# Kernel optimization log

Hardware: AMD Instinct MI355X
Metric: run time of the kernel (lower is better)

Reference implementation:

```python
import jax, jax.numpy as jnp
import numpy as np

DEPTH = 256
HEADS = 8
K = 128          # kernel_size == attended axis length (height)
DH = DEPTH // HEADS  # 32
EPS = 1e-5


def _bn(x, gamma, beta, axes):
    # training-mode batch norm (biased variance), per-channel on axis 1
    mean = jnp.mean(x, axis=axes, keepdims=True)
    var = jnp.var(x, axis=axes, keepdims=True)
    shape = [1] * x.ndim
    shape[1] = x.shape[1]
    g = gamma.reshape(shape)
    b = beta.reshape(shape)
    return (x - mean) * jax.lax.rsqrt(var + EPS) * g + b


def setup_inputs() -> dict:
    key = jax.random.key(0)
    ks = jax.random.split(key, 3)
    x = jax.random.normal(ks[0], (2, DEPTH, K, K), dtype=jnp.float32)
    w_kqv = jax.random.normal(ks[1], (2 * DEPTH, DEPTH), dtype=jnp.float32) * 0.05
    rel_encoding = jax.random.normal(ks[2], (2 * DH, 2 * K - 1), dtype=jnp.float32)
    return {
        "x": x,
        "w_kqv": w_kqv,
        "kqv_gamma": jnp.ones((2 * DEPTH,), jnp.float32),
        "kqv_beta": jnp.zeros((2 * DEPTH,), jnp.float32),
        "logits_gamma": jnp.ones((3 * HEADS,), jnp.float32),
        "logits_beta": jnp.zeros((3 * HEADS,), jnp.float32),
        "rel_encoding": rel_encoding,
    }


def reference(x, w_kqv, kqv_gamma, kqv_beta, logits_gamma, logits_beta, rel_encoding):
    B, C, H, W = x.shape  # height_dim=True path
    # (B,C,H,W) -> (B,W,C,H) -> (B*W, C, H)
    xf = jnp.transpose(x, (0, 3, 1, 2)).reshape(B * W, C, H)
    # 1x1 conv == channel matmul
    kqv = jnp.einsum('oc,bch->boh', w_kqv, xf)  # (BW, 2*depth, H)
    kqv = _bn(kqv, kqv_gamma, kqv_beta, axes=(0, 2))
    kqv = kqv.reshape(B * W, HEADS, 2 * DH, H)
    k = kqv[:, :, : DH // 2]            # (BW, h, dh/2, H)
    q = kqv[:, :, DH // 2: DH]          # (BW, h, dh/2, H)
    v = kqv[:, :, DH:]                  # (BW, h, dh,   H)

    # relative position gather: (2*dh, 2K-1) -> (2*dh, K, K)
    idx = (jnp.arange(K)[None, :] - jnp.arange(K)[:, None] + K - 1).reshape(-1)
    rel = rel_encoding[:, idx].reshape(2 * DH, K, K)
    q_enc = rel[: DH // 2]
    k_enc = rel[DH // 2: DH]
    v_enc = rel[DH:]

    qk = jnp.einsum('bhdx,bhdy->bhxy', q, k)
    qr = jnp.einsum('bhdx,dxy->bhxy', q, q_enc)
    kr = jnp.swapaxes(jnp.einsum('bhdx,dxy->bhxy', k, k_enc), 2, 3)
    logits = jnp.concatenate([qk, qr, kr], axis=1)  # (BW, 3*h, K, K)
    logits = _bn(logits, logits_gamma, logits_beta, axes=(0, 2, 3))
    logits = logits.reshape(B * W, 3, HEADS, H, H).sum(axis=1)
    weights = jax.nn.softmax(logits, axis=3)  # (BW, h, K, K)

    attn = jnp.einsum('bhxy,bhdy->bhdx', weights, v)         # (BW, h, dh, H)
    attn_enc = jnp.einsum('bhxy,dxy->bhdx', weights, v_enc)  # (BW, h, dh, H)
    out = (attn + attn_enc).reshape(B, W, DEPTH, H)  # cat+reshape+sum(dim=-2) == add
    out = jnp.transpose(out, (0, 2, 3, 1))  # (B, depth, H, W)
    return out
```

## Files before the change

kernel.cpp:

```cpp
#include <hip/hip_runtime.h>
#include <hip/hip_bf16.h>

#define H 128
#define NB 256
#define OC 512
#define CIN 256
#define NN 16384
#define EPS 1e-5f

#define EQG_OFF 524288
#define EKG_OFF 589824
#define EVG_OFF 655360

typedef __attribute__((ext_vector_type(4))) float f32x4;
typedef __attribute__((ext_vector_type(8))) short bf16x8;
typedef unsigned short u16x8 __attribute__((ext_vector_type(8)));

__device__ __forceinline__ float bf2f(unsigned short u){
    return __uint_as_float(((unsigned int)u) << 16);
}
__device__ __forceinline__ unsigned short f2bf(float f){
    unsigned int x = __float_as_uint(f);
    return (unsigned short)((x + 0x7fffu + ((x >> 16) & 1u)) >> 16);
}
__device__ __forceinline__ float ldin(const void* p, size_t i, bool f32){
    return f32 ? ((const float*)p)[i] : bf2f(((const unsigned short*)p)[i]);
}
__device__ __forceinline__ short ld_bf16(const void* p, size_t i, bool f32){
    if (f32) return (short)f2bf(((const float*)p)[i]);
    return ((const short*)p)[i];
}
__device__ __forceinline__ bool probe_f32(const void* gamma_ones){
    return *(const unsigned int*)gamma_ones == 0x3F800000u;
}

template<bool F32>
__device__ __forceinline__ void gemm_body(const void* __restrict__ w,
                                          const void* __restrict__ x,
                                          unsigned short* __restrict__ c1,
                                          short (*As)[128][40], short (*Bs)[64][40])
{
    const int m0 = blockIdx.x * 128;
    const int n0 = blockIdx.y * 64;
    const int b0 = blockIdx.z;
    const int t  = threadIdx.x;
    const int lane = t & 63, wv = t >> 6;
    const int wm = wv & 1, wn = wv >> 1;
    const int lm = lane & 15, quad = lane >> 4;
    const size_t xb = (size_t)b0 * CIN * NN;
    const int am = t >> 1, ak = (t & 1) * 16;
    const int bn = t & 63, bk = (t >> 6) * 8;

    float4 pa[4]; float pb[8];
    u16x8 qa[2]; unsigned short qb[8];

    auto load_tile = [&](int k0){
        if constexpr (F32){
            const float* wp = (const float*)w + (size_t)(m0+am)*CIN + k0 + ak;
            #pragma unroll
            for (int q=0;q<4;q++) pa[q] = *(const float4*)(wp + 4*q);
            const float* xp = (const float*)x + xb + (size_t)(k0+bk)*NN + n0 + bn;
            #pragma unroll
            for (int i=0;i<8;i++) pb[i] = xp[(size_t)i*NN];
        } else {
            const unsigned short* wp = (const unsigned short*)w + (size_t)(m0+am)*CIN + k0 + ak;
            qa[0] = *(const u16x8*)wp; qa[1] = *(const u16x8*)(wp+8);
            const unsigned short* xp = (const unsigned short*)x + xb + (size_t)(k0+bk)*NN + n0 + bn;
            #pragma unroll
            for (int i=0;i<8;i++) qb[i] = xp[(size_t)i*NN];
        }
    };
    auto store_tile = [&](int buf){
        if constexpr (F32){
            short ta[16];
            #pragma unroll
            for (int q=0;q<4;q++){
                ta[4*q+0]=(short)f2bf(pa[q].x); ta[4*q+1]=(short)f2bf(pa[q].y);
                ta[4*q+2]=(short)f2bf(pa[q].z); ta[4*q+3]=(short)f2bf(pa[q].w);
            }
            *(bf16x8*)&As[buf][am][ak]   = *(bf16x8*)&ta[0];
            *(bf16x8*)&As[buf][am][ak+8] = *(bf16x8*)&ta[8];
            #pragma unroll
            for (int i=0;i<8;i++) Bs[buf][bn][bk+i] = (short)f2bf(pb[i]);
        } else {
            *(u16x8*)&As[buf][am][ak]   = qa[0];
            *(u16x8*)&As[buf][am][ak+8] = qa[1];
            #pragma unroll
            for (int i=0;i<8;i++) Bs[buf][bn][bk+i] = (short)qb[i];
        }
    };

    f32x4 acc[4][2];
    #pragma unroll
    for (int i=0;i<4;i++){ acc[i][0]=(f32x4){0,0,0,0}; acc[i][1]=(f32x4){0,0,0,0}; }

    load_tile(0); store_tile(0); __syncthreads();
    for (int kk=0; kk<8; ++kk){
        const int cur = kk & 1;
        if (kk < 7) load_tile((kk+1)*32);
        bf16x8 af[4], bfB[2];
        #pragma unroll
        for (int i=0;i<4;i++) af[i]  = *(const bf16x8*)&As[cur][wm*64 + i*16 + lm][quad*8];
        #pragma unroll
        for (int j=0;j<2;j++) bfB[j] = *(const bf16x8*)&Bs[cur][wn*32 + j*16 + lm][quad*8];
        #pragma unroll
        for (int i=0;i<4;i++)
            #pragma unroll
            for (int j=0;j<2;j++)
                acc[i][j] = __builtin_amdgcn_mfma_f32_16x16x32_bf16(af[i], bfB[j], acc[i][j], 0,0,0);
        if (kk < 7) store_tile(cur ^ 1);
        __syncthreads();
    }
    #pragma unroll
    for (int i=0;i<4;i++){
        #pragma unroll
        for (int j=0;j<2;j++){
            int n = n0 + wn*32 + j*16 + lm;
            #pragma unroll
            for (int r=0;r<4;r++){
                int m = m0 + wm*64 + i*16 + quad*4 + r;
                c1[((size_t)b0*OC + m)*NN + n] = f2bf(acc[i][j][r]);
            }
        }
    }
}

__global__ __launch_bounds__(256) void k_gemm(const void* __restrict__ w,
                                              const void* __restrict__ x,
                                              unsigned short* __restrict__ c1,
                                              const void* __restrict__ probe)
{
    __shared__ short As[2][128][40];
    __shared__ short Bs[2][64][40];
    if (probe_f32(probe)) gemm_body<true >(w, x, c1, As, Bs);
    else                  gemm_body<false>(w, x, c1, As, Bs);
}

__global__ __launch_bounds__(256) void k_bn_transpose(const unsigned short* __restrict__ c1,
        unsigned short* __restrict__ kqvt,
        const void* __restrict__ gamma, const void* __restrict__ beta)
{
    __shared__ float T[128][129];
    __shared__ float red[8];
    __shared__ float sc_sh[2];
    const bool f32 = probe_f32(gamma);
    const int o = blockIdx.x;
    const int t = threadIdx.x;
    const int lane = t & 63, wv = t >> 6;
    const unsigned short* r0 = c1 + (size_t)o*NN;
    const unsigned short* r1 = c1 + ((size_t)OC + o)*NN;
    const u16x8* r08 = (const u16x8*)r0;
    const u16x8* r18 = (const u16x8*)r1;
    float s=0.f, ss=0.f;
    #pragma unroll
    for (int i=0;i<8;i++){
        u16x8 a = r08[t + i*256];
        u16x8 b = r18[t + i*256];
        #pragma unroll
        for (int e=0;e<8;e++){
            float va = bf2f(a[e]); s += va; ss = fmaf(va,va,ss);
            float vb = bf2f(b[e]); s += vb; ss = fmaf(vb,vb,ss);
        }
    }
    #pragma unroll
    for (int off=1; off<64; off<<=1){ s += __shfl_xor(s,off); ss += __shfl_xor(ss,off); }
    if (lane==0){ red[wv*2] = s; red[wv*2+1] = ss; }
    __syncthreads();
    if (t==0){
        float st=0.f, sq=0.f;
        for (int i=0;i<4;i++){ st += red[i*2]; sq += red[i*2+1]; }
        float mean = st * (1.f/32768.f);
        float var  = sq * (1.f/32768.f) - mean*mean;
        float scale = ldin(gamma, o, f32) * rsqrtf(var + EPS);
        sc_sh[0] = scale;
        sc_sh[1] = ldin(beta, o, f32) - mean*scale;
    }
    __syncthreads();
    const float scale = sc_sh[0], shift = sc_sh[1];
    for (int b0=0;b0<2;b0++){
        const unsigned short* r = b0 ? r1 : r0;
        for (int i=0;i<64;i++){
            int idx = t + i*256;
            int h = idx >> 7, ww = idx & 127;
            T[ww][h] = fmaf(bf2f(r[idx]), scale, shift);
        }
        __syncthreads();
        for (int i=0;i<64;i++){
            int idx = t + i*256;
            int ww = idx >> 7, h = idx & 127;
            kqvt[(((size_t)(b0*128 + ww))*OC + o)*H + h] = f2bf(T[ww][h]);
        }
        __syncthreads();
    }
}

__global__ __launch_bounds__(256) void k_encpre(const void* __restrict__ relenc,
        float* __restrict__ ws, const void* __restrict__ probe)
{
    __shared__ float E[16][256];
    const bool f32 = probe_f32(probe);
    const int grp = blockIdx.x;
    const int t = threadIdx.x;
    if (grp == 2){
        unsigned short* ev = (unsigned short*)ws + EVG_OFF;
        for (int i = t; i < 32*264; i += 256){
            int d = i / 264, j = i - d*264;
            ev[i] = (j < 255) ? (unsigned short)ld_bf16(relenc, (size_t)(32+d)*255 + j, f32) : 0;
        }
        return;
    }
    for (int i = t; i < 16*255; i += 256){
        int d = i / 255, j = i - d*255;
        E[d][j] = bf2f((unsigned short)ld_bf16(relenc, (size_t)(grp*16 + d)*255 + j, f32));
    }
    __syncthreads();
    float* Rout = ws + 256  + grp*2048;
    float* Cout = ws + 8192 + grp*32768;
    {
        const int d = t >> 4, e = t & 15;
        const float* Ed = E[d]; const float* Ee = E[e];
        float c = 0.f;
        for (int j = 0; j < 128; ++j) c = fmaf(Ed[j], Ee[j], c);
        float* Cp = Cout + (d*16+e)*128;
        Cp[127] = c;
        for (int xx = 126; xx >= 0; --xx){
            c += Ed[254-xx]*Ee[254-xx] - Ed[126-xx]*Ee[126-xx];
            Cp[xx] = c;
        }
    }
    if (t < 16){
        const float* Ed = E[t];
        float r = 0.f;
        for (int j = 0; j < 128; ++j) r += Ed[j];
        float* Rp = Rout + t*128;
        Rp[127] = r;
        for (int xx = 126; xx >= 0; --xx){
            r += Ed[254-xx] - Ed[126-xx];
            Rp[xx] = r;
        }
    }
}

__global__ __launch_bounds__(256) void k_stats2(const unsigned short* __restrict__ kqvt,
        const float* __restrict__ ws, float* __restrict__ stats)
{
    __shared__ short QK[2][16][128];
    __shared__ float wr[4][6];
    const int b = blockIdx.x >> 3, head = blockIdx.x & 7;
    const int t = threadIdx.x;
    const int lane = t & 63, wv = t >> 6;
    const int lm = lane & 15, quad = lane >> 4;
    const unsigned short* base = kqvt + ((size_t)b*OC + head*64)*H;
    for (int i = t; i < 512; i += 256){
        int arr = i >> 8, d = (i >> 4) & 15, c = i & 15;
        *(u16x8*)&QK[arr][d][c*8] = *(const u16x8*)&base[(size_t)(arr*16 + d)*H + c*8];
    }
    __syncthreads();

    float s_qk = 0.f, q_qk = 0.f;
    if (wv == 0){
        f32x4 gq  = (f32x4){0,0,0,0}, gk  = (f32x4){0,0,0,0};
        f32x4 gq1 = (f32x4){0,0,0,0}, gk1 = (f32x4){0,0,0,0};
        bf16x8 ones;
        #pragma unroll
        for (int i=0;i<8;i++) ones[i] = (short)0x3F80;
        #pragma unroll
        for (int xt=0; xt<4; ++xt){
            bf16x8 fq = *(const bf16x8*)&QK[1][lm][xt*32 + quad*8];
            bf16x8 fk = *(const bf16x8*)&QK[0][lm][xt*32 + quad*8];
            gq  = __builtin_amdgcn_mfma_f32_16x16x32_bf16(fq, fq,   gq,  0,0,0);
            gk  = __builtin_amdgcn_mfma_f32_16x16x32_bf16(fk, fk,   gk,  0,0,0);
            gq1 = __builtin_amdgcn_mfma_f32_16x16x32_bf16(fq, ones, gq1, 0,0,0);
            gk1 = __builtin_amdgcn_mfma_f32_16x16x32_bf16(fk, ones, gk1, 0,0,0);
        }
        #pragma unroll
        for (int r=0;r<4;r++) q_qk += gq[r]*gk[r];
        if (lm == 0){
            #pragma unroll
            for (int r=0;r<4;r++) s_qk += gq1[r]*gk1[r];
        }
    }

    const int half = t >> 7;
    const int x = t & 127;
    float col[16];
    #pragma unroll
    for (int d=0; d<16; ++d) col[d] = bf2f((unsigned short)QK[1-half][d][x]);
    const float* Rp = ws + 256  + half*2048;
    const float* Cp = ws + 8192 + half*32768;
    float sr = 0.f, q2 = 0.f;
    #pragma unroll
    for (int d=0; d<16; ++d) sr = fmaf(col[d], Rp[d*128 + x], sr);
    for (int d=0; d<16; ++d){
        float qd = col[d];
        #pragma unroll
        for (int e=0; e<16; ++e)
            q2 = fmaf(qd*col[e], Cp[(d*16+e)*128 + x], q2);
    }
    float s_qr = half ? 0.f : sr,  q_qr = half ? 0.f : q2;
    float s_kr = half ? sr : 0.f,  q_kr = half ? q2 : 0.f;

    #pragma unroll
    for (int off=1; off<64; off<<=1){
        s_qk += __shfl_xor(s_qk,off); q_qk += __shfl_xor(q_qk,off);
        s_qr += __shfl_xor(s_qr,off); q_qr += __shfl_xor(q_qr,off);
        s_kr += __shfl_xor(s_kr,off); q_kr += __shfl_xor(q_kr,off);
    }
    if (lane==0){ wr[wv][0]=s_qk; wr[wv][1]=s_qr; wr[wv][2]=s_kr;
                  wr[wv][3]=q_qk; wr[wv][4]=q_qr; wr[wv][5]=q_kr; }
    __syncthreads();
    if (t==0){
        float a0=0,a1=0,a2=0,b0_=0,b1=0,b2=0;
        for (int i=0;i<4;i++){ a0+=wr[i][0]; a1+=wr[i][1]; a2+=wr[i][2];
                               b0_+=wr[i][3]; b1+=wr[i][4]; b2+=wr[i][5]; }
        atomicAdd(&stats[head],      a0);
        atomicAdd(&stats[8+head],    a1);
        atomicAdd(&stats[16+head],   a2);
        atomicAdd(&stats[24+head],   b0_);
        atomicAdd(&stats[32+head],   b1);
        atomicAdd(&stats[40+head],   b2);
    }
}

__global__ void k_scales(const float* __restrict__ stats, float* __restrict__ scales,
                         const void* __restrict__ gamma_l, const void* __restrict__ probe)
{
    const bool f32 = probe_f32(probe);
    int t = threadIdx.x;
    if (t < 24){
        const float inv_cnt = 1.f/4194304.f;
        float mean = stats[t]*inv_cnt;
        float var  = stats[24+t]*inv_cnt - mean*mean;
        scales[t] = ldin(gamma_l, t, f32) * rsqrtf(var + EPS);
    }
}

__global__ void k_escale(const void* __restrict__ relenc, const float* __restrict__ scales,
                         unsigned short* __restrict__ etab, const void* __restrict__ probe)
{
    const bool f32 = probe_f32(probe);
    const int head = blockIdx.x;
    const int t = threadIdx.x;
    const float s1 = scales[8+head], s2 = scales[16+head];
    unsigned short* eq = etab + EQG_OFF + head*8192;
    unsigned short* ek = etab + EKG_OFF + head*8192;
    for (int i = t; i < 8192; i += 256){
        int j = i >> 5, c = i & 31;
        unsigned short vq = 0, vk = 0;
        if (c < 16 && j < 255){
            vq = f2bf(s1 * ldin(relenc, (size_t)c*255 + j, f32));
            vk = f2bf(s2 * ldin(relenc, (size_t)(16+c)*255 + j, f32));
        }
        eq[i] = vq; ek[i] = vk;
    }
}

struct SA {
    short QA[128][24];
    short KA[128][24];
};
struct SV {
    short Vs[32][136];
};
union SU { SA a; SV v; };

__global__ __launch_bounds__(256) void k_attn(const unsigned short* __restrict__ kqvt,
        const unsigned short* __restrict__ etab,
        const float* __restrict__ scales,
        void* __restrict__ outp,
        const void* __restrict__ probe)
{
    __shared__ SU smu;
    __shared__ short RW[128][136];
    __shared__ alignas(16) short ZED[16];
    const bool f32 = probe_f32(probe);
    const int blk = blockIdx.x;
    const int b = blk >> 3, head = blk & 7;
    const int b0 = b >> 7, w = b & 127;
    const int t = threadIdx.x;
    const int lane = t & 63, wv = t >> 6;
    const int lm = lane & 15, quad = lane >> 4;
    const unsigned short* base = kqvt + ((size_t)b*OC + head*64)*H;
    const float s0 = scales[head];
    const unsigned short* EQg = etab + EQG_OFF + (size_t)head*8192;
    const unsigned short* EKg = etab + EKG_OFF + (size_t)head*8192;
    const unsigned short* EVg = etab + EVG_OFF;

    {
        int dd = t & 15, xg = (t >> 4) * 8;
        u16x8 kv = *(const u16x8*)&base[dd*H + xg];
        u16x8 qv = *(const u16x8*)&base[(16+dd)*H + xg];
        #pragma unroll
        for (int e=0;e<8;e++){
            smu.a.QA[xg+e][dd] = (short)qv[e];
            smu.a.KA[xg+e][dd] = (short)kv[e];
        }
    }
    if (t < 16) ZED[t] = 0;
    __syncthreads();

    f32x4 qacc[2][8];
    bf16x8 aq[2], akk[2];
    #pragma unroll
    for (int u=0;u<2;u++){
        const int mt = 2*wv + u;
        const short* pa  = (quad < 2) ? &smu.a.QA[mt*16 + lm][quad*8] : &ZED[0];
        const short* pk0 = (quad < 2) ? &smu.a.KA[mt*16 + lm][quad*8] : &ZED[0];
        aq[u]  = *(const bf16x8*)pa;
        akk[u] = *(const bf16x8*)pk0;
        #pragma unroll
        for (int yt=0; yt<8; ++yt){
            const short* pb = (quad < 2) ? &smu.a.KA[yt*16 + lm][quad*8] : &ZED[0];
            bf16x8 bk = *(const bf16x8*)pb;
            qacc[u][yt] = __builtin_amdgcn_mfma_f32_16x16x32_bf16(aq[u], bk,
                            (f32x4){0.f,0.f,0.f,0.f}, 0,0,0);
        }
        for (int jt=0; jt<16; ++jt){
            int sdiag = mt + jt;
            if (sdiag < 7 || sdiag > 15) continue;
            bf16x8 bq = *(const bf16x8*)&EQg[(size_t)(jt*16 + lm)*32 + quad*8];
            f32x4 cq = __builtin_amdgcn_mfma_f32_16x16x32_bf16(aq[u], bq,
                         (f32x4){0.f,0.f,0.f,0.f}, 0,0,0);
            int j = jt*16 + lm;
            #pragma unroll
            for (int r=0;r<4;r++){
                int x = mt*16 + quad*4 + r;
                int y = x + j - 127;
                if ((unsigned)y < 128u) RW[x][y] = (short)f2bf(cq[r]);
            }
        }
    }
    __syncthreads();

    {
        int dd = t & 31, yg = (t >> 5) * 16;
        u16x8 v0 = *(const u16x8*)&base[(32+dd)*H + yg];
        u16x8 v1 = *(const u16x8*)&base[(32+dd)*H + yg + 8];
        *(u16x8*)&smu.v.Vs[dd][yg]   = v0;
        *(u16x8*)&smu.v.Vs[dd][yg+8] = v1;
    }
    #pragma unroll
    for (int u=0;u<2;u++){
        const int mt = 2*wv + u;
        for (int jt=0; jt<16; ++jt){
            int sdiag = mt + jt;
            if (sdiag < 7 || sdiag > 15) continue;
            bf16x8 bkE = *(const bf16x8*)&EKg[(size_t)(jt*16 + lm)*32 + quad*8];
            f32x4 ck = __builtin_amdgcn_mfma_f32_16x16x32_bf16(akk[u], bkE,
                         (f32x4){0.f,0.f,0.f,0.f}, 0,0,0);
            int j = jt*16 + lm;
            #pragma unroll
            for (int r=0;r<4;r++){
                int y = mt*16 + quad*4 + r;
                int x = y + j - 127;
                if ((unsigned)x < 128u){
                    float cur = bf2f((unsigned short)RW[x][y]);
                    RW[x][y] = (short)f2bf(cur + ck[r]);
                }
            }
        }
    }
    __syncthreads();

    #pragma unroll
    for (int u=0;u<2;u++){
        const int mt = 2*wv + u;
        #pragma unroll
        for (int r=0;r<4;r++){
            const int x = mt*16 + quad*4 + r;
            float v[8]; float mx = -1e30f;
            #pragma unroll
            for (int yt=0; yt<8; ++yt){
                v[yt] = fmaf(s0, qacc[u][yt][r], bf2f((unsigned short)RW[x][yt*16 + lm]));
                mx = fmaxf(mx, v[yt]);
            }
            mx = fmaxf(mx, __shfl_xor(mx,1));
            mx = fmaxf(mx, __shfl_xor(mx,2));
            mx = fmaxf(mx, __shfl_xor(mx,4));
            mx = fmaxf(mx, __shfl_xor(mx,8));
            float sum = 0.f;
            #pragma unroll
            for (int yt=0; yt<8; ++yt){ v[yt] = __expf(v[yt]-mx); sum += v[yt]; }
            sum += __shfl_xor(sum,1);
            sum += __shfl_xor(sum,2);
            sum += __shfl_xor(sum,4);
            sum += __shfl_xor(sum,8);
            float inv = 1.f/sum;
            #pragma unroll
            for (int yt=0; yt<8; ++yt)
                RW[x][yt*16 + lm] = (short)f2bf(v[yt]*inv);
        }
    }
    __syncthreads();

    f32x4 o[2][2];
    #pragma unroll
    for (int u=0;u<2;u++){ o[u][0]=(f32x4){0,0,0,0}; o[u][1]=(f32x4){0,0,0,0}; }
    #pragma unroll
    for (int kt=0; kt<4; ++kt){
        bf16x8 bv0 = *(const bf16x8*)&smu.v.Vs[lm][kt*32 + quad*8];
        bf16x8 bv1 = *(const bf16x8*)&smu.v.Vs[16+lm][kt*32 + quad*8];
        #pragma unroll
        for (int u=0;u<2;u++){
            bf16x8 aw = *(const bf16x8*)&RW[(2*wv+u)*16 + lm][kt*32 + quad*8];
            o[u][0] = __builtin_amdgcn_mfma_f32_16x16x32_bf16(aw, bv0, o[u][0], 0,0,0);
            o[u][1] = __builtin_amdgcn_mfma_f32_16x16x32_bf16(aw, bv1, o[u][1], 0,0,0);
        }
    }
    for (int kt=0; kt<8; ++kt){
        bf16x8 be0 = *(const bf16x8*)&EVg[(size_t)lm*264      + kt*32 + quad*8];
        bf16x8 be1 = *(const bf16x8*)&EVg[(size_t)(16+lm)*264 + kt*32 + quad*8];
        #pragma unroll
        for (int u=0;u<2;u++){
            const int mt = 2*wv + u;
            int lo = mt*16 + kt*32 - 127;
            if (lo > 127 || lo + 46 < 0) continue;
            int xg = mt*16 + lm;
            int y0 = xg + kt*32 + quad*8 - 127;
            short g[8];
            #pragma unroll
            for (int jj=0;jj<8;jj++){
                int y = y0 + jj;
                g[jj] = ((unsigned)y < 128u) ? RW[xg][y] : (short)0;
            }
            bf16x8 ag = *(bf16x8*)g;
            o[u][0] = __builtin_amdgcn_mfma_f32_16x16x32_bf16(ag, be0, o[u][0], 0,0,0);
            o[u][1] = __builtin_amdgcn_mfma_f32_16x16x32_bf16(ag, be1, o[u][1], 0,0,0);
        }
    }
    #pragma unroll
    for (int u=0;u<2;u++){
        #pragma unroll
        for (int nt=0; nt<2; ++nt){
            int d = nt*16 + lm;
            size_t cb = ((size_t)(b0*256 + head*32 + d))*16384 + (size_t)w;
            #pragma unroll
            for (int r=0;r<4;r++){
                int x = (2*wv+u)*16 + quad*4 + r;
                if (f32) ((float*)outp)[cb + (size_t)x*128] = o[u][nt][r];
                else ((unsigned short*)outp)[cb + (size_t)x*128] = f2bf(o[u][nt][r]);
            }
        }
    }
}

extern "C" void kernel_launch(void* const* d_in, const int* in_sizes, int n_in,
                              void* d_out, int out_size, void* d_ws, size_t ws_size,
                              hipStream_t stream)
{
    (void)in_sizes; (void)n_in; (void)out_size;
    const void* x      = d_in[0];
    const void* w_kqv  = d_in[1];
    const void* kqv_g  = d_in[2];
    const void* kqv_b  = d_in[3];
    const void* log_g  = d_in[4];
    const void* relenc = d_in[6];

    if (ws_size < (size_t)64*1024*1024) return;
    unsigned short* C1   = (unsigned short*)d_ws;
    unsigned short* KQVT = C1 + 16777216;
    float* WS     = (float*)d_ws;
    float* STATS  = WS;
    float* SCALES = WS + 48;
    unsigned short* ETAB = (unsigned short*)d_ws;

    dim3 g1(OC/128, NN/64, 2);
    k_gemm<<<g1, 256, 0, stream>>>(w_kqv, x, C1, kqv_g);
    k_bn_transpose<<<512, 256, 0, stream>>>(C1, KQVT, kqv_g, kqv_b);
    hipMemsetAsync(STATS, 0, 48*sizeof(float), stream);
    k_encpre<<<3, 256, 0, stream>>>(relenc, WS, kqv_g);
    k_stats2<<<2048, 256, 0, stream>>>(KQVT, WS, STATS);
    k_scales<<<1, 64, 0, stream>>>(STATS, SCALES, log_g, kqv_g);
    k_escale<<<8, 256, 0, stream>>>(relenc, SCALES, ETAB, kqv_g);
    k_attn<<<2048, 256, 0, stream>>>(KQVT, ETAB, SCALES, d_out, kqv_g);
}
```

Before: 369.1 us.

## Fuse BN channel statistics into GEMM epilogue and vectorize transpose

The GEMM epilogue now reduces per-channel sum and sum-of-squares with lane shuffles and atomically adds them into a scratch buffer placed in the output tensor. This removes the separate statistics pass over C1 in the batch-norm transpose kernel. The transpose now uses vectorized 8-wide bf16 loads and stores through a bf16 shared tile, and the float-to-bf16 conversion uses a hardware cvt instruction. The attention kernel loads Q fragments and V operands directly from global memory instead of staging them through shared memory. The costs are atomic contention, reuse of the output buffer as scratch, and statistics computed from fp32 accumulators rather than from rounded bf16 values.

```diff
diff --git a/kernel.cpp b/kernel.cpp
--- a/kernel.cpp
+++ b/kernel.cpp
@@ -20,8 +20,9 @@
     return __uint_as_float(((unsigned int)u) << 16);
 }
 __device__ __forceinline__ unsigned short f2bf(float f){
-    unsigned int x = __float_as_uint(f);
-    return (unsigned short)((x + 0x7fffu + ((x >> 16) & 1u)) >> 16);
+    unsigned int r;
+    asm("v_cvt_pk_bf16_f32 %0, %1, %2" : "=v"(r) : "v"(f), "v"(f));
+    return (unsigned short)r;
 }
 __device__ __forceinline__ float ldin(const void* p, size_t i, bool f32){
     return f32 ? ((const float*)p)[i] : bf2f(((const unsigned short*)p)[i]);
@@ -38,6 +39,7 @@
 __device__ __forceinline__ void gemm_body(const void* __restrict__ w,
                                           const void* __restrict__ x,
                                           unsigned short* __restrict__ c1,
+                                          float* __restrict__ cstats,
                                           short (*As)[128][40], short (*Bs)[64][40])
 {
     const int m0 = blockIdx.x * 128;
@@ -123,54 +125,50 @@
             }
         }
     }
+    #pragma unroll
+    for (int i=0;i<4;i++){
+        #pragma unroll
+        for (int r=0;r<4;r++){
+            float s  = acc[i][0][r] + acc[i][1][r];
+            float ss = fmaf(acc[i][0][r], acc[i][0][r], acc[i][1][r]*acc[i][1][r]);
+            #pragma unroll
+            for (int off=1; off<16; off<<=1){
+                s += __shfl_xor(s, off); ss += __shfl_xor(ss, off);
+            }
+            if (lm == 0){
+                int m = m0 + wm*64 + i*16 + quad*4 + r;
+                atomicAdd(&cstats[2*m],   s);
+                atomicAdd(&cstats[2*m+1], ss);
+            }
+        }
+    }
 }
 
 __global__ __launch_bounds__(256) void k_gemm(const void* __restrict__ w,
                                               const void* __restrict__ x,
                                               unsigned short* __restrict__ c1,
+                                              float* __restrict__ cstats,
                                               const void* __restrict__ probe)
 {
     __shared__ short As[2][128][40];
     __shared__ short Bs[2][64][40];
-    if (probe_f32(probe)) gemm_body<true >(w, x, c1, As, Bs);
-    else                  gemm_body<false>(w, x, c1, As, Bs);
+    if (probe_f32(probe)) gemm_body<true >(w, x, c1, cstats, As, Bs);
+    else                  gemm_body<false>(w, x, c1, cstats, As, Bs);
 }
 
 __global__ __launch_bounds__(256) void k_bn_transpose(const unsigned short* __restrict__ c1,
         unsigned short* __restrict__ kqvt,
-        const void* __restrict__ gamma, const void* __restrict__ beta)
-{
-    __shared__ float T[128][129];
-    __shared__ float red[8];
+        const void* __restrict__ gamma, const void* __restrict__ beta,
+        const float* __restrict__ cstats)
+{
+    __shared__ short T[128][130];
     __shared__ float sc_sh[2];
     const bool f32 = probe_f32(gamma);
     const int o = blockIdx.x;
     const int t = threadIdx.x;
-    const int lane = t & 63, wv = t >> 6;
-    const unsigned short* r0 = c1 + (size_t)o*NN;
-    const unsigned short* r1 = c1 + ((size_t)OC + o)*NN;
-    const u16x8* r08 = (const u16x8*)r0;
-    const u16x8* r18 = (const u16x8*)r1;
-    float s=0.f, ss=0.f;
-    #pragma unroll
-    for (int i=0;i<8;i++){
-        u16x8 a = r08[t + i*256];
-        u16x8 b = r18[t + i*256];
-        #pragma unroll
-        for (int e=0;e<8;e++){
-            float va = bf2f(a[e]); s += va; ss = fmaf(va,va,ss);
-            float vb = bf2f(b[e]); s += vb; ss = fmaf(vb,vb,ss);
-        }
-    }
-    #pragma unroll
-    for (int off=1; off<64; off<<=1){ s += __shfl_xor(s,off); ss += __shfl_xor(ss,off); }
-    if (lane==0){ red[wv*2] = s; red[wv*2+1] = ss; }
-    __syncthreads();
     if (t==0){
-        float st=0.f, sq=0.f;
-        for (int i=0;i<4;i++){ st += red[i*2]; sq += red[i*2+1]; }
-        float mean = st * (1.f/32768.f);
-        float var  = sq * (1.f/32768.f) - mean*mean;
+        float mean = cstats[2*o]   * (1.f/32768.f);
+        float var  = cstats[2*o+1] * (1.f/32768.f) - mean*mean;
         float scale = ldin(gamma, o, f32) * rsqrtf(var + EPS);
         sc_sh[0] = scale;
         sc_sh[1] = ldin(beta, o, f32) - mean*scale;
@@ -178,17 +176,27 @@
     __syncthreads();
     const float scale = sc_sh[0], shift = sc_sh[1];
     for (int b0=0;b0<2;b0++){
-        const unsigned short* r = b0 ? r1 : r0;
-        for (int i=0;i<64;i++){
-            int idx = t + i*256;
-            int h = idx >> 7, ww = idx & 127;
-            T[ww][h] = fmaf(bf2f(r[idx]), scale, shift);
+        const u16x8* r8 = (const u16x8*)(c1 + ((size_t)(b0*OC) + o)*NN);
+        #pragma unroll
+        for (int i=0;i<8;i++){
+            int vi = t + i*256;
+            u16x8 a = r8[vi];
+            int n0_ = vi*8;
+            int h = n0_ >> 7, ww = n0_ & 127;
+            #pragma unroll
+            for (int e=0;e<8;e++) T[ww+e][h] = (short)a[e];
         }
         __syncthreads();
-        for (int i=0;i<64;i++){
-            int idx = t + i*256;
-            int ww = idx >> 7, h = idx & 127;
-            kqvt[(((size_t)(b0*128 + ww))*OC + o)*H + h] = f2bf(T[ww][h]);
+        #pragma unroll
+        for (int i=0;i<8;i++){
+            int vi = t + i*256;
+            int ww = vi >> 4, h8 = (vi & 15)*8;
+            u16x8 tv = *(const u16x8*)&T[ww][h8];
+            unsigned short outv[8];
+            #pragma unroll
+            for (int e=0;e<8;e++)
+                outv[e] = f2bf(fmaf(bf2f((unsigned short)tv[e]), scale, shift));
+            *(u16x8*)&kqvt[(((size_t)(b0*128 + ww))*OC + o)*H + h8] = *(u16x8*)outv;
         }
         __syncthreads();
     }
@@ -355,23 +363,14 @@
     }
 }
 
-struct SA {
-    short QA[128][24];
-    short KA[128][24];
-};
-struct SV {
-    short Vs[32][136];
-};
-union SU { SA a; SV v; };
-
 __global__ __launch_bounds__(256) void k_attn(const unsigned short* __restrict__ kqvt,
         const unsigned short* __restrict__ etab,
         const float* __restrict__ scales,
         void* __restrict__ outp,
         const void* __restrict__ probe)
 {
-    __shared__ SU smu;
-    __shared__ short RW[128][136];
+    __shared__ short KA[128][24];
+    __shared__ short RW[128][134];
     __shared__ alignas(16) short ZED[16];
     const bool f32 = probe_f32(probe);
     const int blk = blockIdx.x;
@@ -389,28 +388,37 @@
     {
         int dd = t & 15, xg = (t >> 4) * 8;
         u16x8 kv = *(const u16x8*)&base[dd*H + xg];
-        u16x8 qv = *(const u16x8*)&base[(16+dd)*H + xg];
-        #pragma unroll
-        for (int e=0;e<8;e++){
-            smu.a.QA[xg+e][dd] = (short)qv[e];
-            smu.a.KA[xg+e][dd] = (short)kv[e];
+        #pragma unroll
+        for (int e=0;e<8;e++) KA[xg+e][dd] = (short)kv[e];
+    }
+    bf16x8 aq[2];
+    #pragma unroll
+    for (int u=0;u<2;u++){
+        aq[u] = (bf16x8){0,0,0,0,0,0,0,0};
+        if (quad < 2){
+            const int x = (2*wv+u)*16 + lm;
+            const unsigned short* qp = base + (16+quad*8)*H + x;
+            #pragma unroll
+            for (int e=0;e<8;e++) aq[u][e] = (short)qp[(size_t)e*H];
         }
     }
     if (t < 16) ZED[t] = 0;
     __syncthreads();
 
+    bf16x8 akk[2];
+    #pragma unroll
+    for (int u=0;u<2;u++){
+        akk[u] = (bf16x8){0,0,0,0,0,0,0,0};
+        if (quad < 2) akk[u] = *(const bf16x8*)&KA[(2*wv+u)*16 + lm][quad*8];
+    }
+
     f32x4 qacc[2][8];
-    bf16x8 aq[2], akk[2];
     #pragma unroll
     for (int u=0;u<2;u++){
         const int mt = 2*wv + u;
-        const short* pa  = (quad < 2) ? &smu.a.QA[mt*16 + lm][quad*8] : &ZED[0];
-        const short* pk0 = (quad < 2) ? &smu.a.KA[mt*16 + lm][quad*8] : &ZED[0];
-        aq[u]  = *(const bf16x8*)pa;
-        akk[u] = *(const bf16x8*)pk0;
         #pragma unroll
         for (int yt=0; yt<8; ++yt){
-            const short* pb = (quad < 2) ? &smu.a.KA[yt*16 + lm][quad*8] : &ZED[0];
+            const short* pb = (quad < 2) ? &KA[yt*16 + lm][quad*8] : &ZED[0];
             bf16x8 bk = *(const bf16x8*)pb;
             qacc[u][yt] = __builtin_amdgcn_mfma_f32_16x16x32_bf16(aq[u], bk,
                             (f32x4){0.f,0.f,0.f,0.f}, 0,0,0);
@@ -432,13 +440,6 @@
     }
     __syncthreads();
 
-    {
-        int dd = t & 31, yg = (t >> 5) * 16;
-        u16x8 v0 = *(const u16x8*)&base[(32+dd)*H + yg];
-        u16x8 v1 = *(const u16x8*)&base[(32+dd)*H + yg + 8];
-        *(u16x8*)&smu.v.Vs[dd][yg]   = v0;
-        *(u16x8*)&smu.v.Vs[dd][yg+8] = v1;
-    }
     #pragma unroll
     for (int u=0;u<2;u++){
         const int mt = 2*wv + u;
@@ -498,8 +499,8 @@
     for (int u=0;u<2;u++){ o[u][0]=(f32x4){0,0,0,0}; o[u][1]=(f32x4){0,0,0,0}; }
     #pragma unroll
     for (int kt=0; kt<4; ++kt){
-        bf16x8 bv0 = *(const bf16x8*)&smu.v.Vs[lm][kt*32 + quad*8];
-        bf16x8 bv1 = *(const bf16x8*)&smu.v.Vs[16+lm][kt*32 + quad*8];
+        bf16x8 bv0 = *(const bf16x8*)&base[(size_t)(32+lm)*H + kt*32 + quad*8];
+        bf16x8 bv1 = *(const bf16x8*)&base[(size_t)(48+lm)*H + kt*32 + quad*8];
         #pragma unroll
         for (int u=0;u<2;u++){
             bf16x8 aw = *(const bf16x8*)&RW[(2*wv+u)*16 + lm][kt*32 + quad*8];
@@ -563,10 +564,12 @@
     float* STATS  = WS;
     float* SCALES = WS + 48;
     unsigned short* ETAB = (unsigned short*)d_ws;
-
+    float* CSTATS = (float*)d_out;
+
+    hipMemsetAsync(CSTATS, 0, 1024*sizeof(float), stream);
     dim3 g1(OC/128, NN/64, 2);
-    k_gemm<<<g1, 256, 0, stream>>>(w_kqv, x, C1, kqv_g);
-    k_bn_transpose<<<512, 256, 0, stream>>>(C1, KQVT, kqv_g, kqv_b);
+    k_gemm<<<g1, 256, 0, stream>>>(w_kqv, x, C1, CSTATS, kqv_g);
+    k_bn_transpose<<<512, 256, 0, stream>>>(C1, KQVT, kqv_g, kqv_b, CSTATS);
     hipMemsetAsync(STATS, 0, 48*sizeof(float), stream);
     k_encpre<<<3, 256, 0, stream>>>(relenc, WS, kqv_g);
     k_stats2<<<2048, 256, 0, stream>>>(KQVT, WS, STATS);
```

Result: slower. 574.9 us (+55.8%).
